# Optimization experiments

Hardware: AMD Instinct MI355X
Metric: run time of the kernel (lower is better)

The kernel has to match this reference:

```python
import jax, jax.numpy as jnp
import numpy as np

DENSITY = 0.1  # fraction of nonzero weights kept by the mask


def setup_inputs() -> dict:
    key = jax.random.key(0)
    k_data, k_w, k_m, k_b = jax.random.split(key, 4)
    M, N, K = 8192, 4096, 4096  # tokens, out_features, in_features
    data = jax.random.normal(k_data, (M, K), dtype=jnp.float32)
    weight = jax.random.normal(k_w, (N, K), dtype=jnp.float32)
    mask = (jax.random.uniform(k_m, (N, K)) < DENSITY).astype(jnp.float32)
    bias = jax.random.normal(k_b, (N,), dtype=jnp.float32)
    return {"data": data, "weight": weight, "mask": mask, "bias": bias}


def reference(data, weight, mask, bias):
    # Equivalent to cuSPARSE CSR SpMM with W_sparse = mask * weight, plus bias:
    # out = data @ (mask * weight)^T + bias  (same math as ref_forward / F.linear)
    w = mask * weight  # [N, K]
    out = jnp.einsum('mk,nk->mn', data, w) + bias  # [M, N]
    return out
```

## Files before the change

### kernel.cpp

```cpp
#include <hip/hip_runtime.h>
#include <hip/hip_bf16.h>


#define Mdim 8192
#define Ndim 4096
#define Kdim 4096

typedef __bf16 bf16x8 __attribute__((ext_vector_type(8)));
typedef float f32x4 __attribute__((ext_vector_type(4)));

__device__ inline unsigned short f2bf(float f) {
    union { float f; unsigned u; } v;
    v.f = f;
    unsigned r = v.u + 0x7fffu + ((v.u >> 16) & 1u);
    return (unsigned short)(r >> 16);
}

__device__ inline unsigned pack2(float a, float b) {
    return (unsigned)f2bf(a) | ((unsigned)f2bf(b) << 16);
}

#define GLOAD_LDS16(gp, lp)                                                     \
    __builtin_amdgcn_global_load_lds((const __attribute__((address_space(1))) void*)(gp), \
                                     (__attribute__((address_space(3))) void*)(lp), 16, 0, 0)

__global__ __launch_bounds__(256) void k_cvt_all(const float4* __restrict__ data,
                                                 const float4* __restrict__ weight,
                                                 const float4* __restrict__ mask,
                                                 uint4* __restrict__ Abf,
                                                 uint4* __restrict__ Bbf) {
    const int NA = Mdim * (Kdim / 8);
    const int NB = Ndim * (Kdim / 8);
    const int stride = gridDim.x * blockDim.x;
    for (int i = blockIdx.x * blockDim.x + threadIdx.x; i < NA + NB; i += stride) {
        if (i < NA) {
            const size_t j2 = 2 * (size_t)i;
            float4 v0 = data[j2], v1 = data[j2 + 1];
            uint4 o;
            o.x = pack2(v0.x, v0.y); o.y = pack2(v0.z, v0.w);
            o.z = pack2(v1.x, v1.y); o.w = pack2(v1.z, v1.w);
            Abf[i] = o;
        } else {
            const size_t j = (size_t)(i - NA);
            const size_t j2 = 2 * j;
            float4 w0 = weight[j2], w1 = weight[j2 + 1];
            float4 m0 = mask[j2],   m1 = mask[j2 + 1];
            uint4 o;
            o.x = pack2(w0.x * m0.x, w0.y * m0.y);
            o.y = pack2(w0.z * m0.z, w0.w * m0.w);
            o.z = pack2(w1.x * m1.x, w1.y * m1.y);
            o.w = pack2(w1.z * m1.z, w1.w * m1.w);
            Bbf[j] = o;
        }
    }
}

__global__ __launch_bounds__(256) void k_gemm(const unsigned short* __restrict__ A,
                                              const unsigned short* __restrict__ B,
                                              const float* __restrict__ bias,
                                              float* __restrict__ out) {
    __shared__ unsigned short As[128 * 32];
    __shared__ unsigned short Bs[128 * 32];

    const int tid  = threadIdx.x;
    const int lane = tid & 63;
    const int wave = tid >> 6;
    const int wm   = (wave >> 1) * 64;
    const int wn   = (wave & 1) * 64;
    const int bm   = blockIdx.y * 128;
    const int bn   = blockIdx.x * 128;

    const int ar = lane >> 2;
    const int ac = (lane & 3) * 8;
    const unsigned short* Ag0 = A + (size_t)(bm + wave * 32 + ar) * Kdim + ac;
    const unsigned short* Ag1 = Ag0 + (size_t)16 * Kdim;
    const unsigned short* Bg0 = B + (size_t)(bn + wave * 32 + ar) * Kdim + ac;
    const unsigned short* Bg1 = Bg0 + (size_t)16 * Kdim;
    unsigned short* Al0 = As + wave * 1024 + lane * 8;
    unsigned short* Al1 = Al0 + 512;
    unsigned short* Bl0 = Bs + wave * 1024 + lane * 8;
    unsigned short* Bl1 = Bl0 + 512;

    f32x4 zero = {0.f, 0.f, 0.f, 0.f};
    f32x4 acc[4][4];
#pragma unroll
    for (int i = 0; i < 4; ++i)
#pragma unroll
        for (int j = 0; j < 4; ++j) acc[i][j] = zero;

    const int fr = lane & 15;
    const int fk = (lane >> 4) * 8;

    for (int k0 = 0; k0 < Kdim; k0 += 32) {
        GLOAD_LDS16(Ag0 + k0, Al0);
        GLOAD_LDS16(Ag1 + k0, Al1);
        GLOAD_LDS16(Bg0 + k0, Bl0);
        GLOAD_LDS16(Bg1 + k0, Bl1);
        __syncthreads();

        bf16x8 af[4], bfr[4];
#pragma unroll
        for (int i = 0; i < 4; ++i)
            af[i] = *(const bf16x8*)&As[(wm + i * 16 + fr) * 32 + fk];
#pragma unroll
        for (int j = 0; j < 4; ++j)
            bfr[j] = *(const bf16x8*)&Bs[(wn + j * 16 + fr) * 32 + fk];

#pragma unroll
        for (int i = 0; i < 4; ++i)
#pragma unroll
            for (int j = 0; j < 4; ++j)
                acc[i][j] = __builtin_amdgcn_mfma_f32_16x16x32_bf16(af[i], bfr[j], acc[i][j], 0, 0, 0);

        __syncthreads();
    }

    const int col_base = bn + wn + (lane & 15);
    const int row_base = bm + wm + (lane >> 4) * 4;
#pragma unroll
    for (int j = 0; j < 4; ++j) {
        const int col = col_base + j * 16;
        const float bv = bias[col];
#pragma unroll
        for (int i = 0; i < 4; ++i) {
            const int row = row_base + i * 16;
            float* op = out + (size_t)row * Ndim + col;
#pragma unroll
            for (int r = 0; r < 4; ++r) op[(size_t)r * Ndim] = acc[i][j][r] + bv;
        }
    }
}

__global__ void k_naive(const float* __restrict__ A, const float* __restrict__ W,
                        const float* __restrict__ Msk, const float* __restrict__ bias,
                        float* __restrict__ out) {
    int n = blockIdx.x * blockDim.x + threadIdx.x;
    int m = blockIdx.y;
    if (n >= Ndim) return;
    const float* a = A + (size_t)m * Kdim;
    const float* w = W + (size_t)n * Kdim;
    const float* mk = Msk + (size_t)n * Kdim;
    float s = 0.f;
    for (int k = 0; k < Kdim; ++k) s += a[k] * w[k] * mk[k];
    out[(size_t)m * Ndim + n] = s + bias[n];
}

extern "C" void kernel_launch(void* const* d_in, const int* in_sizes, int n_in,
                              void* d_out, int out_size, void* d_ws, size_t ws_size,
                              hipStream_t stream) {
    const float* data   = (const float*)d_in[0];
    const float* weight = (const float*)d_in[1];
    const float* mask   = (const float*)d_in[2];
    const float* bias   = (const float*)d_in[3];
    float* out = (float*)d_out;

    const size_t needA = (size_t)Mdim * Kdim * 2;
    const size_t needB = (size_t)Ndim * Kdim * 2;
    if (ws_size < needA + needB) {
        dim3 g((Ndim + 255) / 256, Mdim);
        k_naive<<<g, 256, 0, stream>>>(data, weight, mask, bias, out);
        return;
    }

    unsigned short* Abf = (unsigned short*)d_ws;
    unsigned short* Bbf = Abf + (size_t)Mdim * Kdim;

    k_cvt_all<<<4096, 256, 0, stream>>>((const float4*)data, (const float4*)weight,
                                        (const float4*)mask, (uint4*)Abf, (uint4*)Bbf);

    dim3 grid(Ndim / 128, Mdim / 128);
    k_gemm<<<grid, 256, 0, stream>>>(Abf, Bbf, bias, out);
}
```

Measured before the change: 616.8 us.

## Double GEMM K-step to 64, add XOR-swizzled LDS layout and grouped block raster

The bf16 MFMA GEMM now stages a 64-wide K slice per iteration instead of 32. This halves the number of barrier pairs and loop iterations. The LDS tiles use an XOR swizzle on the 16-byte chunk index to avoid bank conflicts on fragment reads. Blocks are remapped into groups of 8 M-tiles that sweep N, which improves L2 reuse of the A and B tiles. LDS use doubles to 32 KB per block, and the loop is still single-buffered with no overlap of loads and compute.

```diff
diff --git a/kernel.cpp b/kernel.cpp
--- a/kernel.cpp
+++ b/kernel.cpp
@@ -59,27 +59,28 @@
                                               const unsigned short* __restrict__ B,
                                               const float* __restrict__ bias,
                                               float* __restrict__ out) {
-    __shared__ unsigned short As[128 * 32];
-    __shared__ unsigned short Bs[128 * 32];
+    __shared__ unsigned short As[128 * 64];
+    __shared__ unsigned short Bs[128 * 64];
 
     const int tid  = threadIdx.x;
     const int lane = tid & 63;
     const int wave = tid >> 6;
     const int wm   = (wave >> 1) * 64;
     const int wn   = (wave & 1) * 64;
-    const int bm   = blockIdx.y * 128;
-    const int bn   = blockIdx.x * 128;
 
-    const int ar = lane >> 2;
-    const int ac = (lane & 3) * 8;
-    const unsigned short* Ag0 = A + (size_t)(bm + wave * 32 + ar) * Kdim + ac;
-    const unsigned short* Ag1 = Ag0 + (size_t)16 * Kdim;
-    const unsigned short* Bg0 = B + (size_t)(bn + wave * 32 + ar) * Kdim + ac;
-    const unsigned short* Bg1 = Bg0 + (size_t)16 * Kdim;
-    unsigned short* Al0 = As + wave * 1024 + lane * 8;
-    unsigned short* Al1 = Al0 + 512;
-    unsigned short* Bl0 = Bs + wave * 1024 + lane * 8;
-    unsigned short* Bl1 = Bl0 + 512;
+    const int bid = blockIdx.y * gridDim.x + blockIdx.x;
+    const int per_group = 8 * 32;
+    const int gidx = bid / per_group;
+    const int rem  = bid % per_group;
+    const int bm = (gidx * 8 + (rem & 7)) * 128;
+    const int bn = (rem >> 3) * 128;
+
+    const int sr = lane >> 3;
+    const int sc = ((lane & 7) ^ sr) * 8;
+    const unsigned short* Ag = A + (size_t)(bm + wave * 32 + sr) * Kdim + sc;
+    const unsigned short* Bg = B + (size_t)(bn + wave * 32 + sr) * Kdim + sc;
+    unsigned short* Al = As + (wave * 32) * 64 + lane * 8;
+    unsigned short* Bl = Bs + (wave * 32) * 64 + lane * 8;
 
     f32x4 zero = {0.f, 0.f, 0.f, 0.f};
     f32x4 acc[4][4];
@@ -89,29 +90,33 @@
         for (int j = 0; j < 4; ++j) acc[i][j] = zero;
 
     const int fr = lane & 15;
-    const int fk = (lane >> 4) * 8;
+    const int fx = fr & 7;
+    const int g0 = lane >> 4;
 
-    for (int k0 = 0; k0 < Kdim; k0 += 32) {
-        GLOAD_LDS16(Ag0 + k0, Al0);
-        GLOAD_LDS16(Ag1 + k0, Al1);
-        GLOAD_LDS16(Bg0 + k0, Bl0);
-        GLOAD_LDS16(Bg1 + k0, Bl1);
+    for (int k0 = 0; k0 < Kdim; k0 += 64) {
+#pragma unroll
+        for (int c = 0; c < 4; ++c) {
+            GLOAD_LDS16(Ag + k0 + (size_t)(c * 8) * Kdim, Al + c * 512);
+            GLOAD_LDS16(Bg + k0 + (size_t)(c * 8) * Kdim, Bl + c * 512);
+        }
         __syncthreads();
 
-        bf16x8 af[4], bfr[4];
 #pragma unroll
-        for (int i = 0; i < 4; ++i)
-            af[i] = *(const bf16x8*)&As[(wm + i * 16 + fr) * 32 + fk];
+        for (int kh = 0; kh < 2; ++kh) {
+            const int ch = ((g0 + kh * 4) ^ fx) * 8;
+            bf16x8 af[4], bfr[4];
 #pragma unroll
-        for (int j = 0; j < 4; ++j)
-            bfr[j] = *(const bf16x8*)&Bs[(wn + j * 16 + fr) * 32 + fk];
-
-#pragma unroll
-        for (int i = 0; i < 4; ++i)
+            for (int i = 0; i < 4; ++i)
+                af[i] = *(const bf16x8*)&As[(wm + i * 16 + fr) * 64 + ch];
 #pragma unroll
             for (int j = 0; j < 4; ++j)
-                acc[i][j] = __builtin_amdgcn_mfma_f32_16x16x32_bf16(af[i], bfr[j], acc[i][j], 0, 0, 0);
-
+                bfr[j] = *(const bf16x8*)&Bs[(wn + j * 16 + fr) * 64 + ch];
+#pragma unroll
+            for (int i = 0; i < 4; ++i)
+#pragma unroll
+                for (int j = 0; j < 4; ++j)
+                    acc[i][j] = __builtin_amdgcn_mfma_f32_16x16x32_bf16(af[i], bfr[j], acc[i][j], 0, 0, 0);
+        }
         __syncthreads();
     }
 
```

New measurement: 667.3 us. 8.2% more time.
